# Kernel optimization log

Measured on AMD Instinct MI355X. Metric: run time of the kernel, lower is better.

The kernel has to match this reference:

```python
import jax, jax.numpy as jnp
import numpy as np

B, SEQ, D_TOK = 2, 2048, 1536
H, DH = 24, 64
TP, NS, NMH, DFLOW = 4, 256, 8, 64


def setup_inputs() -> dict:
    key = jax.random.key(0)
    ks = jax.random.split(key, 10)
    s = 0.02  # weight scale to keep activations sane
    return {
        "hidden_states": jax.random.normal(ks[0], (B, SEQ, D_TOK), jnp.float32),
        "Wq": jax.random.normal(ks[1], (D_TOK, D_TOK), jnp.float32) * s,
        "Wk": jax.random.normal(ks[2], (D_TOK, D_TOK), jnp.float32) * s,
        "Wv": jax.random.normal(ks[3], (D_TOK, D_TOK), jnp.float32) * s,
        "Wo": jax.random.normal(ks[4], (D_TOK, D_TOK), jnp.float32) * s,
        "bo": jnp.zeros((D_TOK,), jnp.float32),
        "M": jax.random.normal(ks[5], (B, TP, NS, DFLOW), jnp.float32),
        "W_region": jax.random.uniform(ks[6], (B, TP, NS, 1), jnp.float32),
        "Fk": jax.random.normal(ks[7], (NMH, DFLOW, DH), jnp.float32) * s,
        "Fv": jax.random.normal(ks[8], (NMH, DFLOW, DH), jnp.float32) * s,
    }


def reference(hidden_states, Wq, Wk, Wv, Wo, bo, M, W_region, Fk, Fv):
    # QKV projections, split into heads: [B, H, seq, Dh]
    Q = (hidden_states @ Wq).reshape(B, SEQ, H, DH).transpose(0, 2, 1, 3)
    K = (hidden_states @ Wk).reshape(B, SEQ, H, DH).transpose(0, 2, 1, 3)
    V = (hidden_states @ Wv).reshape(B, SEQ, H, DH).transpose(0, 2, 1, 3)

    # Motion injection (vectorized over b, h, t): region-gated flow deltas
    # delta[b,h,t,n,d] = W_region[b,t,n] * (M[b,t,n,:] @ Fk[h])
    gate = W_region[:, None]  # [B,1,TP,NS,1]
    dK = jnp.einsum('btnf,hfd->bhtnd', M, Fk) * gate  # [B,NMH,TP,NS,DH]
    dV = jnp.einsum('btnf,hfd->bhtnd', M, Fv) * gate

    # seq = 2 blocks (content, canny) x TP frames x NS spatial tokens;
    # delta is applied to both halves of each frame, first NMH heads only.
    K = K.reshape(B, H, 2, TP, NS, DH).at[:, :NMH].add(dK[:, :, None]).reshape(B, H, SEQ, DH)
    V = V.reshape(B, H, 2, TP, NS, DH).at[:, :NMH].add(dV[:, :, None]).reshape(B, H, SEQ, DH)

    # Standard SDPA
    scale = 1.0 / np.sqrt(DH).astype(np.float32)
    scores = jnp.einsum('bhqd,bhkd->bhqk', Q, K) * scale
    attn_w = jax.nn.softmax(scores, axis=-1)
    out = jnp.einsum('bhqk,bhkd->bhqd', attn_w, V)

    out = out.transpose(0, 2, 1, 3).reshape(B, SEQ, D_TOK)
    return out @ Wo + bo
```

## Files before the change

kernel.cpp:

```cpp
#include <hip/hip_runtime.h>
#include <hip/hip_bf16.h>

typedef __attribute__((ext_vector_type(4))) float f32x4;
typedef __attribute__((ext_vector_type(8))) short bf16x8;

#define LOG2E 1.4426950408889634f

__device__ __forceinline__ unsigned short f2b(float f) {
  union { float f; unsigned u; } v; v.f = f;
  unsigned r = v.u + 0x7fffu + ((v.u >> 16) & 1u);
  return (unsigned short)(r >> 16);
}
__device__ __forceinline__ float b2f(unsigned short s) {
  union { unsigned u; float f; } v; v.u = ((unsigned)s) << 16;
  return v.f;
}
__device__ __forceinline__ unsigned cvtpk(float lo, float hi) {
  unsigned r;
  asm("v_cvt_pk_bf16_f32 %0, %1, %2" : "=v"(r) : "v"(lo), "v"(hi));
  return r;
}
__device__ __forceinline__ float fexp2(float x) {
  float r;
  asm("v_exp_f32 %0, %1" : "=v"(r) : "v"(x));
  return r;
}
__device__ __forceinline__ void gload_lds16(const void* g, void* l) {
  __builtin_amdgcn_global_load_lds(
      (const __attribute__((address_space(1))) unsigned*)g,
      (__attribute__((address_space(3))) unsigned*)l, 16, 0, 0);
}
__device__ __forceinline__ f32x4 mfma16(bf16x8 a, bf16x8 b, f32x4 c) {
  return __builtin_amdgcn_mfma_f32_16x16x32_bf16(a, b, c, 0, 0, 0);
}

__global__ __launch_bounds__(256) void k_cvt(const float* __restrict__ src,
                                             unsigned short* __restrict__ dst, int n4) {
  int i = blockIdx.x * 256 + threadIdx.x;
  if (i >= n4) return;
  float4 v = ((const float4*)src)[i];
  ushort4 o;
  o.x = f2b(v.x); o.y = f2b(v.y); o.z = f2b(v.z); o.w = f2b(v.w);
  ((ushort4*)dst)[i] = o;
}

__global__ __launch_bounds__(256) void k_transpose3(const float* __restrict__ s0,
                                                    const float* __restrict__ s1,
                                                    const float* __restrict__ s2,
                                                    unsigned short* __restrict__ dst) {
  __shared__ float tile[64][65];
  const int which = blockIdx.x / 576;
  const int bid = blockIdx.x % 576;
  const float* src = which == 0 ? s0 : (which == 1 ? s1 : s2);
  unsigned short* d = dst + (size_t)which * 1536 * 1536;
  const int tx = threadIdx.x & 63, ty = threadIdx.x >> 6;
  const int r0 = (bid / 24) * 64, c0 = (bid % 24) * 64;
#pragma unroll
  for (int j = 0; j < 16; ++j)
    tile[ty + j * 4][tx] = src[(size_t)(r0 + ty + j * 4) * 1536 + c0 + tx];
  __syncthreads();
#pragma unroll
  for (int j = 0; j < 16; ++j)
    d[(size_t)(c0 + ty + j * 4) * 1536 + r0 + tx] = f2b(tile[tx][ty + j * 4]);
}

__global__ __launch_bounds__(256) void k_transpose(const float* __restrict__ src,
                                                   unsigned short* __restrict__ dst) {
  __shared__ float tile[64][65];
  const int tx = threadIdx.x & 63, ty = threadIdx.x >> 6;
  const int r0 = (blockIdx.x / 24) * 64, c0 = (blockIdx.x % 24) * 64;
#pragma unroll
  for (int j = 0; j < 16; ++j)
    tile[ty + j * 4][tx] = src[(size_t)(r0 + ty + j * 4) * 1536 + c0 + tx];
  __syncthreads();
#pragma unroll
  for (int j = 0; j < 16; ++j)
    dst[(size_t)(c0 + ty + j * 4) * 1536 + r0 + tx] = f2b(tile[tx][ty + j * 4]);
}

__global__ __launch_bounds__(512, 2) void k_gemm8(const unsigned short* __restrict__ A,
                                                  const unsigned short* __restrict__ BT,
                                                  unsigned short* __restrict__ C,
                                                  int M, int N, int K, int gridN) {
  extern __shared__ unsigned short lds[];
  unsigned short* As = lds;
  unsigned short* Bs = lds + 32768;
  const int tid = threadIdx.x;
  const int lane = tid & 63, wave = tid >> 6;
  const int wm = wave >> 2, wn = wave & 3;
  const int r15 = lane & 15, g = lane >> 4;
  const int sw = r15 & 7;
  int bid = blockIdx.x;
  {
    int cpx = gridDim.x >> 3;
    bid = (bid & 7) * cpx + (bid >> 3);
  }
  const int bm = (bid / gridN) * 256;
  const int bn = (bid % gridN) * 256;
  const int NT = K >> 6;

  f32x4 acc[8][4] = {};

  auto STAGE = [&](int tl, int part) {
    const bool isB = part >= 2;
    const int half = part & 1;
    const unsigned short* src = isB ? BT : A;
    const int rb = (isB ? bn : bm) + half * 128;
    char* slot = (char*)(isB ? Bs : As) + ((tl & 1) * 2 + half) * 16384;
#pragma unroll
    for (int i = 0; i < 2; ++i) {
      int cid = i * 512 + tid;
      int row = cid >> 3;
      int logc = (cid & 7) ^ (row & 7);
      gload_lds16(src + (size_t)(rb + row) * K + tl * 64 + logc * 8,
                  slot + i * 8192 + wave * 1024);
    }
  };

  STAGE(0, 2); STAGE(0, 3); STAGE(0, 0); STAGE(0, 1);
  STAGE(1, 2); STAGE(1, 3); STAGE(1, 0);
  asm volatile("s_waitcnt vmcnt(6)" ::: "memory");
  __builtin_amdgcn_s_barrier();

  bf16x8 af[4][2], bf[4][2];
  for (int t = 0; t < NT; ++t) {
    const int d = t & 1;
    const unsigned short* Aslot = As + (d * 2 + wm) * 8192;
    const unsigned short* Bslot = Bs + (d * 2 + (wn >> 1)) * 8192;
    const int bro = (wn & 1) * 64;

#pragma unroll
    for (int j = 0; j < 4; ++j) {
      const unsigned short* ar = Aslot + (j * 16 + r15) * 64;
      af[j][0] = *(const bf16x8*)(ar + ((g ^ sw) * 8));
      af[j][1] = *(const bf16x8*)(ar + (((4 + g) ^ sw) * 8));
    }
#pragma unroll
    for (int n = 0; n < 2; ++n) {
      const unsigned short* br = Bslot + (bro + n * 16 + r15) * 64;
      bf[n][0] = *(const bf16x8*)(br + ((g ^ sw) * 8));
      bf[n][1] = *(const bf16x8*)(br + (((4 + g) ^ sw) * 8));
    }
    if (t + 1 < NT) STAGE(t + 1, 1);
    __builtin_amdgcn_s_barrier();
    asm volatile("s_waitcnt lgkmcnt(0)" ::: "memory");
    __builtin_amdgcn_sched_barrier(0);
    __builtin_amdgcn_s_setprio(1);
#pragma unroll
    for (int j = 0; j < 4; ++j)
#pragma unroll
      for (int n = 0; n < 2; ++n) {
        acc[j][n] = mfma16(af[j][0], bf[n][0], acc[j][n]);
        acc[j][n] = mfma16(af[j][1], bf[n][1], acc[j][n]);
      }
    __builtin_amdgcn_s_setprio(0);
    __builtin_amdgcn_s_barrier();

#pragma unroll
    for (int n = 2; n < 4; ++n) {
      const unsigned short* br = Bslot + (bro + n * 16 + r15) * 64;
      bf[n][0] = *(const bf16x8*)(br + ((g ^ sw) * 8));
      bf[n][1] = *(const bf16x8*)(br + (((4 + g) ^ sw) * 8));
    }
    __builtin_amdgcn_s_barrier();
    asm volatile("s_waitcnt lgkmcnt(0)" ::: "memory");
    __builtin_amdgcn_sched_barrier(0);
    __builtin_amdgcn_s_setprio(1);
#pragma unroll
    for (int j = 0; j < 4; ++j)
#pragma unroll
      for (int n = 2; n < 4; ++n) {
        acc[j][n] = mfma16(af[j][0], bf[n][0], acc[j][n]);
        acc[j][n] = mfma16(af[j][1], bf[n][1], acc[j][n]);
      }
    __builtin_amdgcn_s_setprio(0);
    __builtin_amdgcn_s_barrier();

#pragma unroll
    for (int j = 0; j < 4; ++j) {
      const unsigned short* ar = Aslot + (64 + j * 16 + r15) * 64;
      af[j][0] = *(const bf16x8*)(ar + ((g ^ sw) * 8));
      af[j][1] = *(const bf16x8*)(ar + (((4 + g) ^ sw) * 8));
    }
    if (t + 2 < NT) STAGE(t + 2, 2);
    __builtin_amdgcn_s_barrier();
    asm volatile("s_waitcnt lgkmcnt(0)" ::: "memory");
    __builtin_amdgcn_sched_barrier(0);
    __builtin_amdgcn_s_setprio(1);
#pragma unroll
    for (int j = 0; j < 4; ++j)
#pragma unroll
      for (int n = 0; n < 2; ++n) {
        acc[4 + j][n] = mfma16(af[j][0], bf[n][0], acc[4 + j][n]);
        acc[4 + j][n] = mfma16(af[j][1], bf[n][1], acc[4 + j][n]);
      }
    __builtin_amdgcn_s_setprio(0);
    __builtin_amdgcn_s_barrier();

    if (t + 2 < NT) { STAGE(t + 2, 3); STAGE(t + 2, 0); }
    __builtin_amdgcn_s_barrier();
    __builtin_amdgcn_s_setprio(1);
#pragma unroll
    for (int j = 0; j < 4; ++j)
#pragma unroll
      for (int n = 2; n < 4; ++n) {
        acc[4 + j][n] = mfma16(af[j][0], bf[n][0], acc[4 + j][n]);
        acc[4 + j][n] = mfma16(af[j][1], bf[n][1], acc[4 + j][n]);
      }
    __builtin_amdgcn_s_setprio(0);
    if (t < NT - 2)
      asm volatile("s_waitcnt vmcnt(6)" ::: "memory");
    else
      asm volatile("s_waitcnt vmcnt(0)" ::: "memory");
    __builtin_amdgcn_s_barrier();
  }

#pragma unroll
  for (int m = 0; m < 8; ++m)
#pragma unroll
    for (int n = 0; n < 4; ++n)
#pragma unroll
      for (int i = 0; i < 4; ++i) {
        int row = bm + wm * 128 + m * 16 + g * 4 + i;
        int col = bn + wn * 64 + n * 16 + r15;
        C[(size_t)row * N + col] = f2b(acc[m][n][i]);
      }
}

template <int OUTBF16>
__global__ __launch_bounds__(256) void k_gemm(const unsigned short* __restrict__ A,
                                              const unsigned short* __restrict__ BT,
                                              void* __restrict__ C,
                                              const float* __restrict__ bias,
                                              int M, int N, int K, int gridN) {
  __shared__ unsigned short As[128 * 32];
  __shared__ unsigned short Bs[128 * 32];
  const int tid = threadIdx.x;
  const int lane = tid & 63, wave = tid >> 6;
  int bidx = blockIdx.x;
  {
    int cpx = gridDim.x >> 3;
    bidx = (bidx & 7) * cpx + (bidx >> 3);
  }
  const int bm = (bidx / gridN) * 128;
  const int bn = (bidx % gridN) * 128;
  const int wr = (wave >> 1) * 64, wc = (wave & 1) * 64;
  const int r15 = lane & 15, g = lane >> 4;
  const int row0 = tid >> 2, c0 = tid & 3;

  f32x4 acc[4][4] = {};

  for (int k0 = 0; k0 < K; k0 += 32) {
    __syncthreads();
    gload_lds16(A + (size_t)(bm + row0) * K + k0 + c0 * 8, (char*)As + wave * 1024);
    gload_lds16(A + (size_t)(bm + row0 + 64) * K + k0 + c0 * 8,
                (char*)As + 4096 + wave * 1024);
    gload_lds16(BT + (size_t)(bn + row0) * K + k0 + c0 * 8, (char*)Bs + wave * 1024);
    gload_lds16(BT + (size_t)(bn + row0 + 64) * K + k0 + c0 * 8,
                (char*)Bs + 4096 + wave * 1024);
    __syncthreads();
    bf16x8 af[4], bfr[4];
#pragma unroll
    for (int m = 0; m < 4; ++m) {
      af[m] = *(const bf16x8*)&As[(wr + m * 16 + r15) * 32 + g * 8];
      bfr[m] = *(const bf16x8*)&Bs[(wc + m * 16 + r15) * 32 + g * 8];
    }
#pragma unroll
    for (int m = 0; m < 4; ++m)
#pragma unroll
      for (int n = 0; n < 4; ++n)
        acc[m][n] = mfma16(af[m], bfr[n], acc[m][n]);
  }

#pragma unroll
  for (int m = 0; m < 4; ++m)
#pragma unroll
    for (int n = 0; n < 4; ++n)
#pragma unroll
      for (int i = 0; i < 4; ++i) {
        int row = bm + wr + m * 16 + g * 4 + i;
        int col = bn + wc + n * 16 + r15;
        float v = acc[m][n][i];
        if (OUTBF16)
          ((unsigned short*)C)[(size_t)row * N + col] = f2b(v);
        else
          ((float*)C)[(size_t)row * N + col] = v + bias[col];
      }
}

__global__ __launch_bounds__(256) void k_inject(const float* __restrict__ Mm,
                                                const float* __restrict__ Wr,
                                                const float* __restrict__ Fk,
                                                const float* __restrict__ Fv,
                                                unsigned short* __restrict__ qkv) {
  __shared__ float Ml[256];
  __shared__ float gl[4];
  const int bid = blockIdx.x;
  const int nb = bid & 63, t = (bid >> 6) & 3, h = (bid >> 8) & 7, b = bid >> 11;
  const int tid = threadIdx.x;
  const int nl = tid >> 6, d = tid & 63;
  Ml[tid] = Mm[(size_t)(((b * 4 + t) * 256 + nb * 4) * 64) + tid];
  if (tid < 4) gl[tid] = Wr[(b * 4 + t) * 256 + nb * 4 + tid];
  __syncthreads();
  float ak = 0.f, av = 0.f;
#pragma unroll 8
  for (int f = 0; f < 64; ++f) {
    float mv = Ml[nl * 64 + f];
    ak += mv * Fk[(h * 64 + f) * 64 + d];
    av += mv * Fv[(h * 64 + f) * 64 + d];
  }
  float gate = gl[nl];
  ak *= gate; av *= gate;
  const int n = nb * 4 + nl;
  const size_t s0 = (size_t)(b * 2048 + t * 256 + n);
#pragma unroll
  for (int r = 0; r < 2; ++r) {
    size_t row = s0 + (size_t)r * 1024;
    size_t ik = row * 4608 + 1536 + h * 64 + d;
    qkv[ik] = f2b(b2f(qkv[ik]) + ak);
    size_t iv = row * 4608 + 3072 + h * 64 + d;
    qkv[iv] = f2b(b2f(qkv[iv]) + av);
  }
}

__global__ __launch_bounds__(256, 3) void k_attn(const unsigned short* __restrict__ qkv,
                                                 unsigned short* __restrict__ attno) {
  __shared__ unsigned short Kl[2 * 64 * 64];
  __shared__ unsigned short VT[2 * 64 * 72];
  const int tid = threadIdx.x;
  const int lane = tid & 63, wave = tid >> 6;
  const int bid = blockIdx.x;
  const int qt = bid & 15;
  const int h = (bid >> 4) % 24;
  const int b = (bid >> 4) / 24;
  const int r15 = lane & 15, g = lane >> 4;
  const int q0 = qt * 128 + wave * 32;
  const size_t RS = 4608;
  const size_t tokbase = (size_t)(b * 2048);

  bf16x8 qb[2][2];
  {
    const float qs = 0.125f * LOG2E;
#pragma unroll
    for (int qh = 0; qh < 2; ++qh) {
      const unsigned short* qrow = qkv + (tokbase + q0 + qh * 16 + r15) * RS + h * 64;
#pragma unroll
      for (int kk = 0; kk < 2; ++kk) {
        bf16x8 v = *(const bf16x8*)(qrow + kk * 32 + g * 8);
#pragma unroll
        for (int e = 0; e < 8; ++e)
          v[e] = (short)f2b(b2f((unsigned short)v[e]) * qs);
        qb[qh][kk] = v;
      }
    }
  }

  f32x4 o[2][4] = {};
  float m_run[2] = {-1e30f, -1e30f}, l_run[2] = {0.f, 0.f};
  bf16x8 vr[2];

  const int ch0 = wave * 2 * 64 + lane, ch1 = (wave * 2 + 1) * 64 + lane;
  const int kr0 = ch0 >> 3, kc0s = ((ch0 & 7) ^ (kr0 & 7)) * 8;
  const int kr1 = ch1 >> 3, kc1s = ((ch1 & 7) ^ (kr1 & 7)) * 8;
  const int kcol = ((lane >> 5) & 1) * 32 + ((lane >> 2) & 3) * 8 +
                   ((lane >> 4) & 1) * 4 + (lane & 3);

#define STAGE_K(buf, kv0)                                                          \
  {                                                                                \
    gload_lds16(qkv + (tokbase + (kv0) + kr0) * RS + 1536 + h * 64 + kc0s,         \
                (char*)Kl + (buf) * 8192 + (wave * 2) * 1024);                     \
    gload_lds16(qkv + (tokbase + (kv0) + kr1) * RS + 1536 + h * 64 + kc1s,         \
                (char*)Kl + (buf) * 8192 + (wave * 2 + 1) * 1024);                 \
  }
#define LOAD_V(kv0)                                                                \
  {                                                                                \
    const unsigned short* vrow = qkv + (tokbase + (kv0) + lane) * RS + 3072 + h * 64; \
    vr[0] = *(const bf16x8*)(vrow + (wave * 2) * 8);                               \
    vr[1] = *(const bf16x8*)(vrow + (wave * 2 + 1) * 8);                           \
  }
#define WRITE_V(buf)                                                               \
  {                                                                                \
    _Pragma("unroll") for (int s = 0; s < 2; ++s) {                                \
      int d0 = (wave * 2 + s) * 8;                                                 \
      _Pragma("unroll") for (int e = 0; e < 8; ++e)                                \
          VT[(buf) * 4608 + (d0 + e) * 72 + kcol] = (unsigned short)vr[s][e];      \
    }                                                                              \
  }

  STAGE_K(0, 0);
  LOAD_V(0);
  asm volatile("s_waitcnt vmcnt(0)" ::: "memory");
  WRITE_V(0);
  __syncthreads();

  int cur = 0;
  for (int t = 0; t < 32; ++t) {
    const int kv0 = t * 64;
    if (t < 31) {
      STAGE_K(cur ^ 1, kv0 + 64);
      LOAD_V(kv0 + 64);
    }

    f32x4 st[4][2];
    const unsigned short* Kb = Kl + cur * 4096;
    __builtin_amdgcn_s_setprio(1);
#pragma unroll
    for (int m = 0; m < 4; ++m) {
      int row = m * 16 + r15;
      int r7 = row & 7;
      bf16x8 ka0 = *(const bf16x8*)&Kb[row * 64 + ((g ^ r7) * 8)];
      bf16x8 ka1 = *(const bf16x8*)&Kb[row * 64 + (((4 + g) ^ r7) * 8)];
#pragma unroll
      for (int qh = 0; qh < 2; ++qh) {
        f32x4 z = {0.f, 0.f, 0.f, 0.f};
        st[m][qh] = mfma16(ka0, qb[qh][0], z);
        st[m][qh] = mfma16(ka1, qb[qh][1], st[m][qh]);
      }
    }
    __builtin_amdgcn_s_setprio(0);

    float pm[2];
#pragma unroll
    for (int qh = 0; qh < 2; ++qh) {
      float p = fmaxf(fmaxf(fmaxf(st[0][qh][0], st[0][qh][1]), fmaxf(st[0][qh][2], st[0][qh][3])),
                      fmaxf(fmaxf(st[1][qh][0], st[1][qh][1]), fmaxf(st[1][qh][2], st[1][qh][3])));
      p = fmaxf(p,
                fmaxf(fmaxf(fmaxf(st[2][qh][0], st[2][qh][1]), fmaxf(st[2][qh][2], st[2][qh][3])),
                      fmaxf(fmaxf(st[3][qh][0], st[3][qh][1]), fmaxf(st[3][qh][2], st[3][qh][3]))));
      p = fmaxf(p, __shfl_xor(p, 16, 64));
      pm[qh] = fmaxf(p, __shfl_xor(p, 32, 64));
    }

    if (!__all(pm[0] - m_run[0] <= 8.0f && pm[1] - m_run[1] <= 8.0f)) {
#pragma unroll
      for (int qh = 0; qh < 2; ++qh) {
        float mnew = fmaxf(m_run[qh], pm[qh]);
        float fac = fexp2(m_run[qh] - mnew);
        l_run[qh] *= fac;
        float f_i[4];
#pragma unroll
        for (int i = 0; i < 4; ++i)
          f_i[i] = __shfl(fac, (lane & 48) | ((((lane >> 4) & 3) << 2) + i), 64);
#pragma unroll
        for (int dt = 0; dt < 4; ++dt)
#pragma unroll
          for (int i = 0; i < 4; ++i) o[qh][dt][i] *= f_i[i];
        m_run[qh] = mnew;
      }
    }

    unsigned pku[2][4][2];
    float psum[2] = {0.f, 0.f};
#pragma unroll
    for (int m = 0; m < 4; ++m)
#pragma unroll
      for (int qh = 0; qh < 2; ++qh) {
        float p0 = fexp2(st[m][qh][0] - m_run[qh]);
        float p1 = fexp2(st[m][qh][1] - m_run[qh]);
        float p2 = fexp2(st[m][qh][2] - m_run[qh]);
        float p3 = fexp2(st[m][qh][3] - m_run[qh]);
        psum[qh] += (p0 + p1) + (p2 + p3);
        pku[qh][m][0] = cvtpk(p0, p1);
        pku[qh][m][1] = cvtpk(p2, p3);
      }
#pragma unroll
    for (int qh = 0; qh < 2; ++qh) {
      psum[qh] += __shfl_xor(psum[qh], 16, 64);
      psum[qh] += __shfl_xor(psum[qh], 32, 64);
      l_run[qh] += psum[qh];
    }

    const unsigned short* Vb = VT + cur * 4608;
    __builtin_amdgcn_s_setprio(1);
#pragma unroll
    for (int kap = 0; kap < 2; ++kap) {
      union { bf16x8 v; unsigned u[4]; } pa0, pa1;
      pa0.u[0] = pku[0][2 * kap][0];     pa0.u[1] = pku[0][2 * kap][1];
      pa0.u[2] = pku[0][2 * kap + 1][0]; pa0.u[3] = pku[0][2 * kap + 1][1];
      pa1.u[0] = pku[1][2 * kap][0];     pa1.u[1] = pku[1][2 * kap][1];
      pa1.u[2] = pku[1][2 * kap + 1][0]; pa1.u[3] = pku[1][2 * kap + 1][1];
#pragma unroll
      for (int dt = 0; dt < 4; ++dt) {
        bf16x8 vb = *(const bf16x8*)&Vb[(dt * 16 + r15) * 72 + kap * 32 + g * 8];
        o[0][dt] = mfma16(pa0.v, vb, o[0][dt]);
        o[1][dt] = mfma16(pa1.v, vb, o[1][dt]);
      }
    }
    __builtin_amdgcn_s_setprio(0);

    if (t < 31) {
      asm volatile("s_waitcnt vmcnt(0)" ::: "memory");
      WRITE_V(cur ^ 1);
    }
    __syncthreads();
    cur ^= 1;
  }

#pragma unroll
  for (int qh = 0; qh < 2; ++qh) {
    float rl = 1.0f / l_run[qh];
    float r_i[4];
#pragma unroll
    for (int i = 0; i < 4; ++i)
      r_i[i] = __shfl(rl, (lane & 48) | ((((lane >> 4) & 3) << 2) + i), 64);
#pragma unroll
    for (int dt = 0; dt < 4; ++dt)
#pragma unroll
      for (int i = 0; i < 4; ++i) {
        int q = q0 + qh * 16 + ((lane >> 4) << 2) + i;
        int col = h * 64 + dt * 16 + r15;
        attno[(tokbase + q) * 1536 + col] = f2b(o[qh][dt][i] * r_i[i]);
      }
  }
}

extern "C" void kernel_launch(void* const* d_in, const int* in_sizes, int n_in,
                              void* d_out, int out_size, void* d_ws, size_t ws_size,
                              hipStream_t stream) {
  const float* hs = (const float*)d_in[0];
  const float* Wq = (const float*)d_in[1];
  const float* Wk = (const float*)d_in[2];
  const float* Wv = (const float*)d_in[3];
  const float* Wo = (const float*)d_in[4];
  const float* bo = (const float*)d_in[5];
  const float* Mm = (const float*)d_in[6];
  const float* Wr = (const float*)d_in[7];
  const float* Fk = (const float*)d_in[8];
  const float* Fv = (const float*)d_in[9];
  float* out = (float*)d_out;

  unsigned short* hsb   = (unsigned short*)d_ws;
  unsigned short* wqkvt = hsb + (size_t)4096 * 1536;
  unsigned short* qkv   = wqkvt + (size_t)4608 * 1536;
  unsigned short* attno = hsb;
  unsigned short* wot   = wqkvt;

  hipFuncSetAttribute((const void*)k_gemm8,
                      hipFuncAttributeMaxDynamicSharedMemorySize, 131072);

  k_cvt<<<6144, 256, 0, stream>>>(hs, hsb, 1572864);
  k_transpose3<<<1728, 256, 0, stream>>>(Wq, Wk, Wv, wqkvt);

  k_gemm8<<<288, 512, 131072, stream>>>(hsb, wqkvt, qkv, 4096, 4608, 1536, 18);
  k_transpose<<<576, 256, 0, stream>>>(Wo, wot);
  k_inject<<<4096, 256, 0, stream>>>(Mm, Wr, Fk, Fv, qkv);
  k_attn<<<768, 256, 0, stream>>>(qkv, attno);
  k_gemm<0><<<32 * 12, 256, 0, stream>>>(attno, wot, (void*)out, bo, 4096, 1536, 1536, 12);
}
```

Baseline: 243.2 us.

## Split-K the last QKV column tiles to balance the GEMM wave

The QKV GEMM previously launched 288 256x256 tiles, which fills one wave of 256 CUs plus a small tail of 32 tiles. It now runs the first 256 tiles (columns 0-4095) normally and splits the remaining 32 tiles along K into 4 slices each, giving 384 blocks. The slices write fp32 partials to workspace scratch, and a new fixup kernel sums them and stores bf16. The aim is to shorten the tail wave, at the cost of extra scratch traffic and one more kernel launch. The split path only runs if the workspace is large enough.

```diff
diff --git a/kernel.cpp b/kernel.cpp
--- a/kernel.cpp
+++ b/kernel.cpp
@@ -81,7 +81,8 @@
 __global__ __launch_bounds__(512, 2) void k_gemm8(const unsigned short* __restrict__ A,
                                                   const unsigned short* __restrict__ BT,
                                                   unsigned short* __restrict__ C,
-                                                  int M, int N, int K, int gridN) {
+                                                  float* __restrict__ scratch,
+                                                  int K, int gridNmain, int nMain) {
   extern __shared__ unsigned short lds[];
   unsigned short* As = lds;
   unsigned short* Bs = lds + 32768;
@@ -90,30 +91,41 @@
   const int wm = wave >> 2, wn = wave & 3;
   const int r15 = lane & 15, g = lane >> 4;
   const int sw = r15 & 7;
-  int bid = blockIdx.x;
-  {
-    int cpx = gridDim.x >> 3;
+
+  int bm, bn, kbeg, NT, slot;
+  bool partial;
+  if ((int)blockIdx.x < nMain) {
+    int bid = blockIdx.x;
+    int cpx = nMain >> 3;
     bid = (bid & 7) * cpx + (bid >> 3);
-  }
-  const int bm = (bid / gridN) * 256;
-  const int bn = (bid % gridN) * 256;
-  const int NT = K >> 6;
+    bm = (bid / gridNmain) * 256;
+    bn = (bid % gridNmain) * 256;
+    kbeg = 0; NT = K >> 6; partial = false; slot = 0;
+  } else {
+    int s = blockIdx.x - nMain;
+    int tile = s >> 2, slice = s & 3;
+    bm = (tile & 15) * 256;
+    bn = 4096 + (tile >> 4) * 256;
+    kbeg = slice * 384; NT = 6; partial = true; slot = s;
+  }
+  const unsigned short* Ab = A + kbeg;
+  const unsigned short* BTb = BT + kbeg;
 
   f32x4 acc[8][4] = {};
 
   auto STAGE = [&](int tl, int part) {
     const bool isB = part >= 2;
     const int half = part & 1;
-    const unsigned short* src = isB ? BT : A;
+    const unsigned short* src = isB ? BTb : Ab;
     const int rb = (isB ? bn : bm) + half * 128;
-    char* slot = (char*)(isB ? Bs : As) + ((tl & 1) * 2 + half) * 16384;
+    char* slotp = (char*)(isB ? Bs : As) + ((tl & 1) * 2 + half) * 16384;
 #pragma unroll
     for (int i = 0; i < 2; ++i) {
       int cid = i * 512 + tid;
       int row = cid >> 3;
       int logc = (cid & 7) ^ (row & 7);
       gload_lds16(src + (size_t)(rb + row) * K + tl * 64 + logc * 8,
-                  slot + i * 8192 + wave * 1024);
+                  slotp + i * 8192 + wave * 1024);
     }
   };
 
@@ -215,16 +227,51 @@
     __builtin_amdgcn_s_barrier();
   }
 
-#pragma unroll
-  for (int m = 0; m < 8; ++m)
-#pragma unroll
-    for (int n = 0; n < 4; ++n)
-#pragma unroll
-      for (int i = 0; i < 4; ++i) {
-        int row = bm + wm * 128 + m * 16 + g * 4 + i;
-        int col = bn + wn * 64 + n * 16 + r15;
-        C[(size_t)row * N + col] = f2b(acc[m][n][i]);
-      }
+  if (!partial) {
+#pragma unroll
+    for (int m = 0; m < 8; ++m)
+#pragma unroll
+      for (int n = 0; n < 4; ++n)
+#pragma unroll
+        for (int i = 0; i < 4; ++i) {
+          int row = bm + wm * 128 + m * 16 + g * 4 + i;
+          int col = bn + wn * 64 + n * 16 + r15;
+          C[(size_t)row * 4608 + col] = f2b(acc[m][n][i]);
+        }
+  } else {
+    float* sp = scratch + (size_t)slot * 65536;
+#pragma unroll
+    for (int m = 0; m < 8; ++m)
+#pragma unroll
+      for (int n = 0; n < 4; ++n)
+#pragma unroll
+        for (int i = 0; i < 4; ++i) {
+          int rl = wm * 128 + m * 16 + g * 4 + i;
+          int cl = wn * 64 + n * 16 + r15;
+          sp[rl * 256 + cl] = acc[m][n][i];
+        }
+  }
+}
+
+__global__ __launch_bounds__(256) void k_fixup(const float* __restrict__ scratch,
+                                               unsigned short* __restrict__ qkv) {
+  size_t gid = (size_t)blockIdx.x * 256 + threadIdx.x;
+  int tile = (int)(gid >> 14);
+  int elem = (int)(gid & 16383) * 4;
+  const float* base = scratch + (size_t)tile * 4 * 65536;
+  float4 p0 = *(const float4*)(base + elem);
+  float4 p1 = *(const float4*)(base + 65536 + elem);
+  float4 p2 = *(const float4*)(base + 131072 + elem);
+  float4 p3 = *(const float4*)(base + 196608 + elem);
+  ushort4 o;
+  o.x = f2b(p0.x + p1.x + p2.x + p3.x);
+  o.y = f2b(p0.y + p1.y + p2.y + p3.y);
+  o.z = f2b(p0.z + p1.z + p2.z + p3.z);
+  o.w = f2b(p0.w + p1.w + p2.w + p3.w);
+  int r = elem >> 8, c = elem & 255;
+  int row = (tile & 15) * 256 + r;
+  int col = 4096 + (tile >> 4) * 256 + c;
+  *(ushort4*)&qkv[(size_t)row * 4608 + col] = o;
 }
 
 template <int OUTBF16>
@@ -535,13 +582,23 @@
   unsigned short* attno = hsb;
   unsigned short* wot   = wqkvt;
 
+  const size_t base_bytes = ((size_t)4096 * 1536 + (size_t)4608 * 1536 +
+                             (size_t)4096 * 4608) * 2;
+  float* scratch = (float*)((char*)d_ws + base_bytes);
+  const bool split = ws_size >= base_bytes + (size_t)128 * 65536 * 4;
+
   hipFuncSetAttribute((const void*)k_gemm8,
                       hipFuncAttributeMaxDynamicSharedMemorySize, 131072);
 
   k_cvt<<<6144, 256, 0, stream>>>(hs, hsb, 1572864);
   k_transpose3<<<1728, 256, 0, stream>>>(Wq, Wk, Wv, wqkvt);
 
-  k_gemm8<<<288, 512, 131072, stream>>>(hsb, wqkvt, qkv, 4096, 4608, 1536, 18);
+  if (split) {
+    k_gemm8<<<384, 512, 131072, stream>>>(hsb, wqkvt, qkv, scratch, 1536, 16, 256);
+    k_fixup<<<2048, 256, 0, stream>>>(scratch, qkv);
+  } else {
+    k_gemm8<<<288, 512, 131072, stream>>>(hsb, wqkvt, qkv, (float*)nullptr, 1536, 18, 288);
+  }
   k_transpose<<<576, 256, 0, stream>>>(Wo, wot);
   k_inject<<<4096, 256, 0, stream>>>(Mm, Wr, Fk, Fv, qkv);
   k_attn<<<768, 256, 0, stream>>>(qkv, attno);
```

After: 226.3 us. 6.9% less time.
